# Kernel tuning notes

Measured on AMD Instinct MI355X. Metric: run time of the kernel, lower is better.

The kernel has to match this reference:

```python
import jax, jax.numpy as jnp
import numpy as np

N_NODES = 50000
N_EDGES = 600000
D = 128
NEG_SLOPE = (1.0 / 8.0 + 1.0 / 3.0) / 2.0  # RReLU in eval mode: mean of (lower, upper)


def setup_inputs() -> dict:
    key = jax.random.key(0)
    ks = jax.random.split(key, 16)
    inp = {
        'node_feats': jax.random.normal(ks[0], (N_NODES, D), dtype=jnp.float32),
        'edge_feats': jax.random.normal(ks[1], (N_EDGES, D), dtype=jnp.float32),
        'src': jax.random.randint(ks[2], (N_EDGES,), 0, N_NODES, dtype=jnp.int32),
        'dst': jax.random.randint(ks[3], (N_EDGES,), 0, N_NODES, dtype=jnp.int32),
    }
    scale = 1.0 / np.sqrt(D)
    i = 4
    for l in range(2):
        for w in (1, 2, 3):
            inp[f'W{w}_l{l}'] = jax.random.uniform(ks[i], (D, D), jnp.float32, -scale, scale); i += 1
            inp[f'b{w}_l{l}'] = jnp.zeros((D,), jnp.float32)
    return inp


def _layer(h, efeat, src, dst, W1, b1, W2, b2, W3, b3):
    # per-edge message: linear1(src_h + edge_h)  [E, D]
    m = (h[src] + efeat) @ W1 + b1
    # attention score per edge: <h_dst, m_e>
    score = jnp.sum(h[dst] * m, axis=-1)  # [E]
    smax = jax.ops.segment_max(score, dst, num_segments=N_NODES)
    smax = jnp.where(jnp.isfinite(smax), smax, 0.0)
    w = jnp.exp(score - smax[dst])  # [E]
    denom = jax.ops.segment_sum(w, dst, num_segments=N_NODES)  # [N]
    wsum = jax.ops.segment_sum(w[:, None] * m, dst, num_segments=N_NODES)  # [N, D]
    neigh = wsum / jnp.maximum(denom, 1e-30)[:, None]
    deg = jax.ops.segment_sum(jnp.ones_like(score), dst, num_segments=N_NODES)
    self_msg = h @ W2 + b2
    iso_msg = h @ W3 + b3
    self_msg = jnp.where((deg == 0)[:, None], iso_msg, self_msg)
    x = self_msg + neigh
    return jnp.where(x >= 0, x, x * NEG_SLOPE)


def reference(node_feats, edge_feats, src, dst,
              W1_l0, b1_l0, W2_l0, b2_l0, W3_l0, b3_l0,
              W1_l1, b1_l1, W2_l1, b2_l1, W3_l1, b3_l1):
    h = _layer(node_feats, edge_feats, src, dst, W1_l0, b1_l0, W2_l0, b2_l0, W3_l0, b3_l0)
    h = _layer(h, edge_feats, src, dst, W1_l1, b1_l1, W2_l1, b2_l1, W3_l1, b3_l1)
    return h
```

## Files before the change

kernel.cpp:

```cpp
#include <hip/hip_runtime.h>


typedef unsigned short u16;
typedef short bf16x8 __attribute__((ext_vector_type(8)));
typedef float f32x4 __attribute__((ext_vector_type(4)));

#define NEG_SLOPE 0.22916666666666666f

__device__ inline float bf2f(u16 h) { return __uint_as_float(((unsigned)h) << 16); }
__device__ inline u16 f2bf(float f) {
  unsigned u = __float_as_uint(f);
  u += 0x7fffu + ((u >> 16) & 1u);
  return (u16)(u >> 16);
}

__global__ __launch_bounds__(256)
void prep_weights(const float* w0, const float* w1, const float* w2,
                  const float* w3, const float* w4, const float* w5,
                  const float* c0, const float* c1, const float* c2,
                  const float* c3, const float* c4, const float* c5,
                  u16* __restrict__ wf, float* __restrict__ bf) {
  int bid = blockIdx.x, tid = threadIdx.x;
  int b = bid >> 3, qc = (bid & 7) * 8;
  const float* Ws[8] = {w0, w1, w2, w3, w4, w5, w0, w3};
  const float* Cs[6] = {c0, c1, c2, c3, c4, c5};
  const float* W = Ws[b];
  const bool tr = (b >= 6);
  u16* out = wf + (size_t)b * 32768;
  #pragma unroll
  for (int qq = 0; qq < 8; ++qq) {
    int fi = tid * 64 + qc + qq;
    int t = fi >> 11, kc = (fi >> 9) & 3, lane = (fi >> 3) & 63, j = fi & 7;
    int k = kc * 32 + (lane >> 4) * 8 + j;
    int n = t * 16 + (lane & 15);
    float w = tr ? W[n * 128 + k] : W[k * 128 + n];
    u16 hi = f2bf(w);
    u16 lo = f2bf(w - bf2f(hi));
    int base = ((t * 4 + kc) * 2) * 512 + lane * 8 + j;
    out[base] = hi;
    out[base + 512] = lo;
  }
  if ((bid & 7) == 0 && b < 6 && tid < 128) bf[b * 128 + tid] = Cs[b][tid];
}

__global__ __launch_bounds__(256)
void hist_k(const int* __restrict__ dst, int* __restrict__ deg, int E) {
  int i = blockIdx.x * 256 + threadIdx.x;
  int stride = gridDim.x * 256;
  for (; i < E; i += stride) atomicAdd(&deg[dst[i]], 1);
}

__global__ __launch_bounds__(256)
void scan1(const int* __restrict__ deg, int* __restrict__ off,
           int* __restrict__ bsum, int N) {
  __shared__ int sh[256];
  int b = blockIdx.x, t = threadIdx.x;
  int base = b * 1024 + t * 4;
  int v[4];
  #pragma unroll
  for (int i = 0; i < 4; ++i) v[i] = (base + i < N) ? deg[base + i] : 0;
  int s = v[0] + v[1] + v[2] + v[3];
  sh[t] = s;
  __syncthreads();
  for (int o = 1; o < 256; o <<= 1) {
    int x = (t >= o) ? sh[t - o] : 0;
    __syncthreads();
    sh[t] += x;
    __syncthreads();
  }
  int run = sh[t] - s;
  #pragma unroll
  for (int i = 0; i < 4; ++i) {
    if (base + i < N) off[base + i] = run;
    run += v[i];
  }
  if (t == 255) bsum[b] = sh[255];
}

__global__ void scan2(int* __restrict__ bsum, int nb) {
  __shared__ int sh[256];
  int t = threadIdx.x;
  int v = (t < nb) ? bsum[t] : 0;
  sh[t] = v;
  __syncthreads();
  for (int o = 1; o < 256; o <<= 1) {
    int x = (t >= o) ? sh[t - o] : 0;
    __syncthreads();
    sh[t] += x;
    __syncthreads();
  }
  if (t < nb) bsum[t] = sh[t] - v;
}

__global__ __launch_bounds__(256)
void scan3(int* __restrict__ off, const int* __restrict__ bsum,
           int* __restrict__ cursor, int N, int E) {
  int i = blockIdx.x * 256 + threadIdx.x;
  if (i < N) {
    int v = off[i] + bsum[i >> 10];
    off[i] = v;
    cursor[i] = v;
  } else if (i == N) {
    off[N] = E;
  }
}

__global__ __launch_bounds__(256)
void scatter_k(const int* __restrict__ dst, const int* __restrict__ src,
               int* __restrict__ cursor, int* __restrict__ eidx,
               int* __restrict__ csrc, int E) {
  int i = blockIdx.x * 256 + threadIdx.x;
  int stride = gridDim.x * 256;
  for (; i < E; i += stride) {
    int p = atomicAdd(&cursor[dst[i]], 1);
    eidx[p] = i;
    csrc[p] = src[i];
  }
}

__global__ __launch_bounds__(256)
void gemm_n3t(const float* __restrict__ A,
              const u16* __restrict__ wfT, const u16* __restrict__ wf2,
              const u16* __restrict__ wf3, const float* __restrict__ biases,
              float* __restrict__ C0, float* __restrict__ C1,
              float* __restrict__ C2, int M) {
  __shared__ u16 ah[64 * 136];
  __shared__ u16 al[64 * 136];
  const int tid = threadIdx.x;
  const long long rowBase = (long long)blockIdx.x * 64;
  #pragma unroll
  for (int it = 0; it < 8; ++it) {
    int idx = it * 256 + tid;
    int row = idx >> 5, c4 = idx & 31;
    long long gr = rowBase + row;
    float4 v = make_float4(0.f, 0.f, 0.f, 0.f);
    if (gr < M) v = ((const float4*)A)[gr * 32 + c4];
    u16 hb[4] = {f2bf(v.x), f2bf(v.y), f2bf(v.z), f2bf(v.w)};
    u16 lb[4] = {f2bf(v.x - bf2f(hb[0])), f2bf(v.y - bf2f(hb[1])),
                 f2bf(v.z - bf2f(hb[2])), f2bf(v.w - bf2f(hb[3]))};
    *(uint2*)&ah[row * 136 + c4 * 4] = *(uint2*)hb;
    *(uint2*)&al[row * 136 + c4 * 4] = *(uint2*)lb;
  }
  __syncthreads();
  const int wid = tid >> 6, lane = tid & 63, lrow = lane & 15, lk = lane >> 4;
  bf16x8 af[4], alf[4];
  #pragma unroll
  for (int kc = 0; kc < 4; ++kc) {
    af[kc]  = *(const bf16x8*)&ah[(wid * 16 + lrow) * 136 + kc * 32 + lk * 8];
    alf[kc] = *(const bf16x8*)&al[(wid * 16 + lrow) * 136 + kc * 32 + lk * 8];
  }
  const u16* wfs[3] = {wfT, wf2, wf3};
  float* Cs[3] = {C0, C1, C2};
  for (int m = 0; m < 3; ++m) {
    const u16* wf = wfs[m];
    float* C = Cs[m];
    f32x4 acc[8];
    #pragma unroll
    for (int t = 0; t < 8; ++t) acc[t] = (f32x4){0.f, 0.f, 0.f, 0.f};
    #pragma unroll
    for (int t = 0; t < 8; ++t) {
      #pragma unroll
      for (int kc = 0; kc < 4; ++kc) {
        bf16x8 bh = *(const bf16x8*)&wf[((t * 4 + kc) * 2) * 512 + lane * 8];
        bf16x8 bl = *(const bf16x8*)&wf[((t * 4 + kc) * 2 + 1) * 512 + lane * 8];
        acc[t] = __builtin_amdgcn_mfma_f32_16x16x32_bf16(af[kc],  bh, acc[t], 0, 0, 0);
        acc[t] = __builtin_amdgcn_mfma_f32_16x16x32_bf16(alf[kc], bh, acc[t], 0, 0, 0);
        acc[t] = __builtin_amdgcn_mfma_f32_16x16x32_bf16(af[kc],  bl, acc[t], 0, 0, 0);
      }
    }
    #pragma unroll
    for (int t = 0; t < 8; ++t) {
      int col = t * 16 + lrow;
      float bv = (m == 1) ? biases[128 + col] : (m == 2) ? biases[256 + col] : 0.f;
      #pragma unroll
      for (int r = 0; r < 4; ++r) {
        long long row = rowBase + wid * 16 + lk * 4 + r;
        if (row < M) C[row * 128 + col] = acc[t][r] + bv;
      }
    }
  }
}

__global__ __launch_bounds__(256)
void edge_agg(const float* __restrict__ efeat, const float* __restrict__ h,
              const float* __restrict__ hT1, const int* __restrict__ off,
              const int* __restrict__ eidx, const int* __restrict__ csrc,
              float* __restrict__ U, int N) {
  int node = blockIdx.x * 4 + (threadIdx.x >> 6);
  if (node >= N) return;
  const int lane = threadIdx.x & 63;
  const size_t nb = (size_t)node * 128 + 2 * lane;
  int s0 = off[node], s1 = off[node + 1];
  if (s1 == s0) {
    *(float2*)&U[nb] = make_float2(0.f, 0.f);
    return;
  }
  const float2 ht = *(const float2*)&hT1[nb];
  float mx = -3.4e38f, den = 0.f, ux = 0.f, uy = 0.f;
  for (int base = s0; base < s1; base += 64) {
    int cnt = s1 - base;
    if (cnt > 64) cnt = 64;
    int me = 0, ms = 0;
    if (lane < cnt) { me = eidx[base + lane]; ms = csrc[base + lane]; }
    int e0 = __shfl(me, 0), sA = __shfl(ms, 0);
    float2 ef = *(const float2*)&efeat[(size_t)e0 * 128 + 2 * lane];
    float2 hs = *(const float2*)&h[(size_t)sA * 128 + 2 * lane];
    for (int j = 0; j < cnt; ++j) {
      float vx = ef.x + hs.x, vy = ef.y + hs.y;
      if (j + 1 < cnt) {
        int e1 = __shfl(me, j + 1), sB = __shfl(ms, j + 1);
        ef = *(const float2*)&efeat[(size_t)e1 * 128 + 2 * lane];
        hs = *(const float2*)&h[(size_t)sB * 128 + 2 * lane];
      }
      float psum = vx * ht.x + vy * ht.y;
      #pragma unroll
      for (int o = 32; o > 0; o >>= 1) psum += __shfl_xor(psum, o);
      if (psum > mx) {
        float r = __expf(mx - psum);
        den *= r; ux *= r; uy *= r;
        mx = psum;
      }
      float w = __expf(psum - mx);
      den += w;
      ux += w * vx; uy += w * vy;
    }
  }
  float inv = 1.f / den;
  *(float2*)&U[nb] = make_float2(ux * inv, uy * inv);
}

__global__ __launch_bounds__(256)
void gemm_fin(const float* __restrict__ A,
              const u16* __restrict__ wf,
              const float* __restrict__ biases,
              const float* __restrict__ y2, const float* __restrict__ y3,
              const int* __restrict__ off, float* __restrict__ C, int M) {
  __shared__ u16 ah[64 * 136];
  __shared__ u16 al[64 * 136];
  const int tid = threadIdx.x;
  const long long rowBase = (long long)blockIdx.x * 64;
  #pragma unroll
  for (int it = 0; it < 8; ++it) {
    int idx = it * 256 + tid;
    int row = idx >> 5, c4 = idx & 31;
    long long gr = rowBase + row;
    float4 v = make_float4(0.f, 0.f, 0.f, 0.f);
    if (gr < M) v = ((const float4*)A)[gr * 32 + c4];
    u16 hb[4] = {f2bf(v.x), f2bf(v.y), f2bf(v.z), f2bf(v.w)};
    u16 lb[4] = {f2bf(v.x - bf2f(hb[0])), f2bf(v.y - bf2f(hb[1])),
                 f2bf(v.z - bf2f(hb[2])), f2bf(v.w - bf2f(hb[3]))};
    *(uint2*)&ah[row * 136 + c4 * 4] = *(uint2*)hb;
    *(uint2*)&al[row * 136 + c4 * 4] = *(uint2*)lb;
  }
  __syncthreads();
  const int wid = tid >> 6, lane = tid & 63, lrow = lane & 15, lk = lane >> 4;
  bf16x8 af[4], alf[4];
  #pragma unroll
  for (int kc = 0; kc < 4; ++kc) {
    af[kc]  = *(const bf16x8*)&ah[(wid * 16 + lrow) * 136 + kc * 32 + lk * 8];
    alf[kc] = *(const bf16x8*)&al[(wid * 16 + lrow) * 136 + kc * 32 + lk * 8];
  }
  f32x4 acc[8];
  #pragma unroll
  for (int t = 0; t < 8; ++t) acc[t] = (f32x4){0.f, 0.f, 0.f, 0.f};
  #pragma unroll
  for (int t = 0; t < 8; ++t) {
    #pragma unroll
    for (int kc = 0; kc < 4; ++kc) {
      bf16x8 bh = *(const bf16x8*)&wf[((t * 4 + kc) * 2) * 512 + lane * 8];
      bf16x8 bl = *(const bf16x8*)&wf[((t * 4 + kc) * 2 + 1) * 512 + lane * 8];
      acc[t] = __builtin_amdgcn_mfma_f32_16x16x32_bf16(af[kc],  bh, acc[t], 0, 0, 0);
      acc[t] = __builtin_amdgcn_mfma_f32_16x16x32_bf16(alf[kc], bh, acc[t], 0, 0, 0);
      acc[t] = __builtin_amdgcn_mfma_f32_16x16x32_bf16(af[kc],  bl, acc[t], 0, 0, 0);
    }
  }
  #pragma unroll
  for (int r = 0; r < 4; ++r) {
    long long row = rowBase + wid * 16 + lk * 4 + r;
    if (row >= M) continue;
    int dg = off[row + 1] - off[row];
    #pragma unroll
    for (int t = 0; t < 8; ++t) {
      int col = t * 16 + lrow;
      size_t o = (size_t)row * 128 + col;
      float v;
      if (dg) v = acc[t][r] + y2[o] + biases[col];
      else    v = y3[o];
      v = v >= 0.f ? v : v * NEG_SLOPE;
      C[o] = v;
    }
  }
}

extern "C" void kernel_launch(void* const* d_in, const int* in_sizes, int n_in,
                              void* d_out, int out_size, void* d_ws, size_t ws_size,
                              hipStream_t stream) {
  const int D = 128;
  const int N = in_sizes[0] / D;
  const int E = in_sizes[1] / D;

  const float* node  = (const float*)d_in[0];
  const float* edgef = (const float*)d_in[1];
  const int* src = (const int*)d_in[2];
  const int* dst = (const int*)d_in[3];

  char* p = (char*)d_ws;
  u16*   wfrag = (u16*)p;   p += (size_t)8 * 32768 * 2;
  float* biasf = (float*)p; p += 4096;
  float* hT1   = (float*)p; p += (size_t)N * 512;
  float* y2    = (float*)p; p += (size_t)N * 512;
  float* y3    = (float*)p; p += (size_t)N * 512;
  float* h1    = (float*)p; p += (size_t)N * 512;
  float* Ub    = (float*)p; p += (size_t)N * 512;
  int* deg     = (int*)p;   p += (size_t)N * 4;
  int* off     = (int*)p;   p += (size_t)(N + 256) * 4;
  int* cursor  = (int*)p;   p += (size_t)N * 4;
  int* bsum    = (int*)p;   p += 1024;
  int* eidx    = (int*)p;   p += (size_t)E * 4;
  int* csrc    = (int*)p;   p += (size_t)E * 4;
  (void)ws_size;

  prep_weights<<<64, 256, 0, stream>>>(
      (const float*)d_in[4],  (const float*)d_in[6],  (const float*)d_in[8],
      (const float*)d_in[10], (const float*)d_in[12], (const float*)d_in[14],
      (const float*)d_in[5],  (const float*)d_in[7],  (const float*)d_in[9],
      (const float*)d_in[11], (const float*)d_in[13], (const float*)d_in[15],
      wfrag, biasf);

  const int gN = (N + 63) / 64;
  const int eB = (E + 255) / 256;
  const int nb = (N + 1023) / 1024;

  hipMemsetAsync(deg, 0, (size_t)N * 4, stream);
  hist_k<<<eB, 256, 0, stream>>>(dst, deg, E);
  scan1<<<nb, 256, 0, stream>>>(deg, off, bsum, N);
  scan2<<<1, 256, 0, stream>>>(bsum, nb);
  scan3<<<(N + 256) / 256, 256, 0, stream>>>(off, bsum, cursor, N, E);
  scatter_k<<<eB, 256, 0, stream>>>(dst, src, cursor, eidx, csrc, E);

  for (int l = 0; l < 2; ++l) {
    const float* h = (l == 0) ? node : h1;
    float* hout = (l == 0) ? h1 : (float*)d_out;
    const u16* wf1 = wfrag + (size_t)(l * 3 + 0) * 32768;
    const u16* wf2 = wfrag + (size_t)(l * 3 + 1) * 32768;
    const u16* wf3 = wfrag + (size_t)(l * 3 + 2) * 32768;
    const u16* wfT = wfrag + (size_t)(6 + l) * 32768;
    const float* bset = biasf + l * 384;

    gemm_n3t<<<gN, 256, 0, stream>>>(h, wfT, wf2, wf3, bset, hT1, y2, y3, N);
    edge_agg<<<(N + 3) / 4, 256, 0, stream>>>(edgef, h, hT1, off, eidx, csrc,
                                              Ub, N);
    gemm_fin<<<gN, 256, 0, stream>>>(Ub, wf1, bset, y2, y3, off, hout, N);
  }
}
```

Before: 892.6 us.

## Process four edges per wave in edge aggregation and skip unused iso GEMM

The edge aggregation kernel now splits each 64-lane wave into four 16-lane groups. Each group handles a different edge, loads 8 floats per lane with nontemporal edge-feature loads, and prefetches indices two steps ahead. An online softmax merges the group maxima and partial sums each step, and the partials are reduced across groups at the end. This cuts the serial per-edge shuffle-reduction chain and raises memory-level parallelism. Separately, the node GEMM skips computing the isolated-node projection for 64-row tiles that contain no zero-degree nodes, which adds an extra pass over the offsets plus a barrier.

Result: faster. 797.7 us (-10.6%).

```diff
diff --git a/kernel.cpp b/kernel.cpp
--- a/kernel.cpp
+++ b/kernel.cpp
@@ -122,12 +122,16 @@
 void gemm_n3t(const float* __restrict__ A,
               const u16* __restrict__ wfT, const u16* __restrict__ wf2,
               const u16* __restrict__ wf3, const float* __restrict__ biases,
+              const int* __restrict__ off,
               float* __restrict__ C0, float* __restrict__ C1,
               float* __restrict__ C2, int M) {
   __shared__ u16 ah[64 * 136];
   __shared__ u16 al[64 * 136];
+  __shared__ int anyDeg0;
   const int tid = threadIdx.x;
   const long long rowBase = (long long)blockIdx.x * 64;
+  if (tid == 0) anyDeg0 = 0;
+  __syncthreads();
   #pragma unroll
   for (int it = 0; it < 8; ++it) {
     int idx = it * 256 + tid;
@@ -141,7 +145,12 @@
     *(uint2*)&ah[row * 136 + c4 * 4] = *(uint2*)hb;
     *(uint2*)&al[row * 136 + c4 * 4] = *(uint2*)lb;
   }
+  if (tid < 64) {
+    long long r = rowBase + tid;
+    if (r < M && off[r + 1] == off[r]) anyDeg0 = 1;
+  }
   __syncthreads();
+  const int nsets = anyDeg0 ? 3 : 2;
   const int wid = tid >> 6, lane = tid & 63, lrow = lane & 15, lk = lane >> 4;
   bf16x8 af[4], alf[4];
   #pragma unroll
@@ -151,7 +160,7 @@
   }
   const u16* wfs[3] = {wfT, wf2, wf3};
   float* Cs[3] = {C0, C1, C2};
-  for (int m = 0; m < 3; ++m) {
+  for (int m = 0; m < nsets; ++m) {
     const u16* wf = wfs[m];
     float* C = Cs[m];
     f32x4 acc[8];
@@ -189,44 +198,83 @@
   int node = blockIdx.x * 4 + (threadIdx.x >> 6);
   if (node >= N) return;
   const int lane = threadIdx.x & 63;
-  const size_t nb = (size_t)node * 128 + 2 * lane;
-  int s0 = off[node], s1 = off[node + 1];
-  if (s1 == s0) {
-    *(float2*)&U[nb] = make_float2(0.f, 0.f);
+  const int g = lane >> 4, cl = lane & 15;
+  const size_t nb = (size_t)node * 128 + (size_t)cl * 8;
+  const int s0 = off[node];
+  const int cnt = off[node + 1] - s0;
+  if (cnt == 0) {
+    if (g == 0) {
+      *(f32x4*)&U[nb]     = (f32x4){0.f, 0.f, 0.f, 0.f};
+      *(f32x4*)&U[nb + 4] = (f32x4){0.f, 0.f, 0.f, 0.f};
+    }
     return;
   }
-  const float2 ht = *(const float2*)&hT1[nb];
-  float mx = -3.4e38f, den = 0.f, ux = 0.f, uy = 0.f;
-  for (int base = s0; base < s1; base += 64) {
-    int cnt = s1 - base;
-    if (cnt > 64) cnt = 64;
-    int me = 0, ms = 0;
-    if (lane < cnt) { me = eidx[base + lane]; ms = csrc[base + lane]; }
-    int e0 = __shfl(me, 0), sA = __shfl(ms, 0);
-    float2 ef = *(const float2*)&efeat[(size_t)e0 * 128 + 2 * lane];
-    float2 hs = *(const float2*)&h[(size_t)sA * 128 + 2 * lane];
-    for (int j = 0; j < cnt; ++j) {
-      float vx = ef.x + hs.x, vy = ef.y + hs.y;
-      if (j + 1 < cnt) {
-        int e1 = __shfl(me, j + 1), sB = __shfl(ms, j + 1);
-        ef = *(const float2*)&efeat[(size_t)e1 * 128 + 2 * lane];
-        hs = *(const float2*)&h[(size_t)sB * 128 + 2 * lane];
-      }
-      float psum = vx * ht.x + vy * ht.y;
-      #pragma unroll
-      for (int o = 32; o > 0; o >>= 1) psum += __shfl_xor(psum, o);
-      if (psum > mx) {
-        float r = __expf(mx - psum);
-        den *= r; ux *= r; uy *= r;
-        mx = psum;
-      }
-      float w = __expf(psum - mx);
-      den += w;
-      ux += w * vx; uy += w * vy;
-    }
+  const f32x4 ht0 = *(const f32x4*)&hT1[nb];
+  const f32x4 ht1 = *(const f32x4*)&hT1[nb + 4];
+  float mx = -3.4e38f, den = 0.f;
+  f32x4 u0 = (f32x4){0.f, 0.f, 0.f, 0.f};
+  f32x4 u1 = (f32x4){0.f, 0.f, 0.f, 0.f};
+  const int nsteps = (cnt + 3) >> 2;
+
+  bool actC = (g < cnt);
+  {
+    int i0 = s0 + (actC ? g : 0);
+    int eC = eidx[i0], sC = csrc[i0];
+    const f32x4* efp = (const f32x4*)(efeat + (size_t)eC * 128) + cl * 2;
+    const f32x4* hp  = (const f32x4*)(h + (size_t)sC * 128) + cl * 2;
+    f32x4 fC0 = __builtin_nontemporal_load(efp);
+    f32x4 fC1 = __builtin_nontemporal_load(efp + 1);
+    f32x4 hC0 = hp[0], hC1 = hp[1];
+
+    int j1 = 4 + g;
+    bool actN = (j1 < cnt);
+    int i1 = s0 + (actN ? j1 : 0);
+    int eN = eidx[i1], sN = csrc[i1];
+
+    for (int k = 0; k < nsteps; ++k) {
+      const f32x4* efn = (const f32x4*)(efeat + (size_t)eN * 128) + cl * 2;
+      const f32x4* hn  = (const f32x4*)(h + (size_t)sN * 128) + cl * 2;
+      f32x4 fN0 = __builtin_nontemporal_load(efn);
+      f32x4 fN1 = __builtin_nontemporal_load(efn + 1);
+      f32x4 hN0 = hn[0], hN1 = hn[1];
+      int j2 = (k + 2) * 4 + g;
+      bool act2 = (j2 < cnt);
+      int i2 = s0 + (act2 ? j2 : 0);
+      int e2 = eidx[i2], s2 = csrc[i2];
+
+      f32x4 v0 = fC0 + hC0, v1 = fC1 + hC1;
+      float ps = v0[0] * ht0[0] + v0[1] * ht0[1] + v0[2] * ht0[2] + v0[3] * ht0[3]
+               + v1[0] * ht1[0] + v1[1] * ht1[1] + v1[2] * ht1[2] + v1[3] * ht1[3];
+      ps += __shfl_xor(ps, 1);
+      ps += __shfl_xor(ps, 2);
+      ps += __shfl_xor(ps, 4);
+      ps += __shfl_xor(ps, 8);
+      float s = actC ? ps : -3.4e38f;
+      float m2 = fmaxf(s, __shfl_xor(s, 16));
+      float m4 = fmaxf(m2, __shfl_xor(m2, 32));
+      float mxn = fmaxf(mx, m4);
+      float r = __expf(mx - mxn);
+      float w = __expf(s - mxn);
+      float w2 = w + __shfl_xor(w, 16);
+      float w4 = w2 + __shfl_xor(w2, 32);
+      den = den * r + w4;
+      u0 = u0 * r + w * v0;
+      u1 = u1 * r + w * v1;
+      mx = mxn;
+      fC0 = fN0; fC1 = fN1; hC0 = hN0; hC1 = hN1; actC = actN;
+      eN = e2; sN = s2; actN = act2;
+    }
+  }
+  #pragma unroll
+  for (int c = 0; c < 4; ++c) {
+    u0[c] += __shfl_xor(u0[c], 16); u0[c] += __shfl_xor(u0[c], 32);
+    u1[c] += __shfl_xor(u1[c], 16); u1[c] += __shfl_xor(u1[c], 32);
   }
   float inv = 1.f / den;
-  *(float2*)&U[nb] = make_float2(ux * inv, uy * inv);
+  if (g == 0) {
+    *(f32x4*)&U[nb]     = u0 * inv;
+    *(f32x4*)&U[nb + 4] = u1 * inv;
+  }
 }
 
 __global__ __launch_bounds__(256)
@@ -347,7 +395,7 @@
     const u16* wfT = wfrag + (size_t)(6 + l) * 32768;
     const float* bset = biasf + l * 384;
 
-    gemm_n3t<<<gN, 256, 0, stream>>>(h, wfT, wf2, wf3, bset, hT1, y2, y3, N);
+    gemm_n3t<<<gN, 256, 0, stream>>>(h, wfT, wf2, wf3, bset, off, hT1, y2, y3, N);
     edge_agg<<<(N + 3) / 4, 256, 0, stream>>>(edgef, h, hT1, off, eidx, csrc,
                                               Ub, N);
     gemm_fin<<<gN, 256, 0, stream>>>(Ub, wf1, bset, y2, y3, off, hout, N);
```

## Restructure edge aggregation to 16 lanes per node with 4-deep prefetch

Applied to the files above, without the earlier changes.

The edge aggregation kernel now assigns 16 lanes per node instead of a full 64-lane wavefront. Each lane handles 8 features with 128-bit loads, and four edges stay in flight through a software-pipelined prefetch ring using nontemporal loads for edge features. The (edge, src) indices are packed into one int2 array so each edge needs a single index load. The node GEMM also skips the isolated-node weight product for tiles with no zero-degree node. The online softmax defers rescaling until the max grows by more than 8, which trades a small risk of reduced exp range for fewer rescales, and packing 4 nodes per wave can cause divergence when degrees differ.

Result: faster. 797.1 us (-10.7%).

```diff
diff --git a/kernel.cpp b/kernel.cpp
--- a/kernel.cpp
+++ b/kernel.cpp
@@ -107,14 +107,12 @@
 
 __global__ __launch_bounds__(256)
 void scatter_k(const int* __restrict__ dst, const int* __restrict__ src,
-               int* __restrict__ cursor, int* __restrict__ eidx,
-               int* __restrict__ csrc, int E) {
+               int* __restrict__ cursor, int2* __restrict__ epair, int E) {
   int i = blockIdx.x * 256 + threadIdx.x;
   int stride = gridDim.x * 256;
   for (; i < E; i += stride) {
     int p = atomicAdd(&cursor[dst[i]], 1);
-    eidx[p] = i;
-    csrc[p] = src[i];
+    epair[p] = make_int2(i, src[i]);
   }
 }
 
@@ -122,12 +120,16 @@
 void gemm_n3t(const float* __restrict__ A,
               const u16* __restrict__ wfT, const u16* __restrict__ wf2,
               const u16* __restrict__ wf3, const float* __restrict__ biases,
+              const int* __restrict__ off,
               float* __restrict__ C0, float* __restrict__ C1,
               float* __restrict__ C2, int M) {
   __shared__ u16 ah[64 * 136];
   __shared__ u16 al[64 * 136];
+  __shared__ int anyDeg0;
   const int tid = threadIdx.x;
   const long long rowBase = (long long)blockIdx.x * 64;
+  if (tid == 0) anyDeg0 = 0;
+  __syncthreads();
   #pragma unroll
   for (int it = 0; it < 8; ++it) {
     int idx = it * 256 + tid;
@@ -141,7 +143,12 @@
     *(uint2*)&ah[row * 136 + c4 * 4] = *(uint2*)hb;
     *(uint2*)&al[row * 136 + c4 * 4] = *(uint2*)lb;
   }
-  __syncthreads();
+  if (tid < 64) {
+    long long r = rowBase + tid;
+    if (r < M && off[r + 1] == off[r]) anyDeg0 = 1;
+  }
+  __syncthreads();
+  const int nsets = anyDeg0 ? 3 : 2;
   const int wid = tid >> 6, lane = tid & 63, lrow = lane & 15, lk = lane >> 4;
   bf16x8 af[4], alf[4];
   #pragma unroll
@@ -151,7 +158,7 @@
   }
   const u16* wfs[3] = {wfT, wf2, wf3};
   float* Cs[3] = {C0, C1, C2};
-  for (int m = 0; m < 3; ++m) {
+  for (int m = 0; m < nsets; ++m) {
     const u16* wf = wfs[m];
     float* C = Cs[m];
     f32x4 acc[8];
@@ -184,49 +191,86 @@
 __global__ __launch_bounds__(256)
 void edge_agg(const float* __restrict__ efeat, const float* __restrict__ h,
               const float* __restrict__ hT1, const int* __restrict__ off,
-              const int* __restrict__ eidx, const int* __restrict__ csrc,
-              float* __restrict__ U, int N) {
-  int node = blockIdx.x * 4 + (threadIdx.x >> 6);
-  if (node >= N) return;
-  const int lane = threadIdx.x & 63;
-  const size_t nb = (size_t)node * 128 + 2 * lane;
-  int s0 = off[node], s1 = off[node + 1];
-  if (s1 == s0) {
-    *(float2*)&U[nb] = make_float2(0.f, 0.f);
-    return;
-  }
-  const float2 ht = *(const float2*)&hT1[nb];
-  float mx = -3.4e38f, den = 0.f, ux = 0.f, uy = 0.f;
-  for (int base = s0; base < s1; base += 64) {
-    int cnt = s1 - base;
-    if (cnt > 64) cnt = 64;
-    int me = 0, ms = 0;
-    if (lane < cnt) { me = eidx[base + lane]; ms = csrc[base + lane]; }
-    int e0 = __shfl(me, 0), sA = __shfl(ms, 0);
-    float2 ef = *(const float2*)&efeat[(size_t)e0 * 128 + 2 * lane];
-    float2 hs = *(const float2*)&h[(size_t)sA * 128 + 2 * lane];
-    for (int j = 0; j < cnt; ++j) {
-      float vx = ef.x + hs.x, vy = ef.y + hs.y;
-      if (j + 1 < cnt) {
-        int e1 = __shfl(me, j + 1), sB = __shfl(ms, j + 1);
-        ef = *(const float2*)&efeat[(size_t)e1 * 128 + 2 * lane];
-        hs = *(const float2*)&h[(size_t)sB * 128 + 2 * lane];
-      }
-      float psum = vx * ht.x + vy * ht.y;
-      #pragma unroll
-      for (int o = 32; o > 0; o >>= 1) psum += __shfl_xor(psum, o);
-      if (psum > mx) {
-        float r = __expf(mx - psum);
-        den *= r; ux *= r; uy *= r;
-        mx = psum;
-      }
-      float w = __expf(psum - mx);
-      den += w;
-      ux += w * vx; uy += w * vy;
-    }
-  }
-  float inv = 1.f / den;
-  *(float2*)&U[nb] = make_float2(ux * inv, uy * inv);
+              const int2* __restrict__ epair, float* __restrict__ U, int N) {
+  const int node = blockIdx.x * 16 + (threadIdx.x >> 4);
+  const int cl = threadIdx.x & 15;
+  const bool valid = (node < N);
+  const size_t nb = (size_t)node * 128 + (size_t)cl * 8;
+  int s0 = 0, cnt = 0;
+  if (valid) {
+    s0 = off[node];
+    cnt = off[node + 1] - s0;
+  }
+  int jm = cnt;
+  jm = max(jm, __shfl_xor(jm, 16));
+  jm = max(jm, __shfl_xor(jm, 32));
+
+  f32x4 ht0 = (f32x4){0.f, 0.f, 0.f, 0.f}, ht1 = ht0;
+  if (valid && cnt > 0) {
+    ht0 = *(const f32x4*)&hT1[nb];
+    ht1 = *(const f32x4*)&hT1[nb + 4];
+  }
+
+  f32x4 fA0, fA1, hA0, hA1, fB0, fB1, hB0, hB1;
+  f32x4 fC0, fC1, hC0, hC1, fD0, fD1, hD0, hD1;
+  int2 iA = make_int2(0, 0), iB = iA, iC = iA, iD = iA;
+
+  #define PRO(S, JJ)                                                          \
+    if (JJ < cnt) {                                                           \
+      int2 pr = epair[s0 + JJ];                                               \
+      const f32x4* efp = (const f32x4*)(efeat + (size_t)pr.x * 128) + cl * 2; \
+      f##S##0 = __builtin_nontemporal_load(efp);                              \
+      f##S##1 = __builtin_nontemporal_load(efp + 1);                          \
+      const f32x4* hp = (const f32x4*)(h + (size_t)pr.y * 128) + cl * 2;      \
+      h##S##0 = hp[0]; h##S##1 = hp[1];                                       \
+      if (JJ + 4 < cnt) i##S = epair[s0 + JJ + 4];                            \
+    }
+  PRO(A, 0) PRO(B, 1) PRO(C, 2) PRO(D, 3)
+  #undef PRO
+
+  float mx = -3.4e38f, den = 0.f;
+  f32x4 u0 = (f32x4){0.f, 0.f, 0.f, 0.f}, u1 = u0;
+
+  #define PROC(S, OFS) {                                                      \
+    int je = j + OFS;                                                         \
+    if (je < cnt) {                                                           \
+      f32x4 v0 = f##S##0 + h##S##0, v1 = f##S##1 + h##S##1;                   \
+      float ps = v0[0]*ht0[0] + v0[1]*ht0[1] + v0[2]*ht0[2] + v0[3]*ht0[3]    \
+               + v1[0]*ht1[0] + v1[1]*ht1[1] + v1[2]*ht1[2] + v1[3]*ht1[3];   \
+      ps += __shfl_xor(ps, 1); ps += __shfl_xor(ps, 2);                       \
+      ps += __shfl_xor(ps, 4); ps += __shfl_xor(ps, 8);                       \
+      if (ps > mx + 8.f) {                                                    \
+        float rr = __expf(mx - ps);           \
+        den *= rr; u0 *= rr; u1 *= rr; mx = ps;                               \
+      }                                                                       \
+      float w = __expf(ps - mx);                          \
+      den += w; u0 += w * v0; u1 += w * v1;                                   \
+      int jr = je + 4;                                                        \
+      if (jr < cnt) {                                                         \
+        const f32x4* efp = (const f32x4*)(efeat + (size_t)i##S.x * 128) + cl * 2; \
+        f##S##0 = __builtin_nontemporal_load(efp);                            \
+        f##S##1 = __builtin_nontemporal_load(efp + 1);                        \
+        const f32x4* hp = (const f32x4*)(h + (size_t)i##S.y * 128) + cl * 2;  \
+        h##S##0 = hp[0]; h##S##1 = hp[1];                                     \
+        if (je + 8 < cnt) i##S = epair[s0 + je + 8];                          \
+      }                                                                       \
+    }                                                                         \
+  }
+  for (int j = 0; j < jm; j += 4) {
+    PROC(A, 0) PROC(B, 1) PROC(C, 2) PROC(D, 3)
+  }
+  #undef PROC
+
+  if (valid) {
+    if (cnt == 0) {
+      *(f32x4*)&U[nb]     = (f32x4){0.f, 0.f, 0.f, 0.f};
+      *(f32x4*)&U[nb + 4] = (f32x4){0.f, 0.f, 0.f, 0.f};
+    } else {
+      float inv = 1.f / den;
+      *(f32x4*)&U[nb]     = u0 * inv;
+      *(f32x4*)&U[nb + 4] = u1 * inv;
+    }
+  }
 }
 
 __global__ __launch_bounds__(256)
@@ -316,8 +360,7 @@
   int* off     = (int*)p;   p += (size_t)(N + 256) * 4;
   int* cursor  = (int*)p;   p += (size_t)N * 4;
   int* bsum    = (int*)p;   p += 1024;
-  int* eidx    = (int*)p;   p += (size_t)E * 4;
-  int* csrc    = (int*)p;   p += (size_t)E * 4;
+  int2* epair  = (int2*)p;  p += (size_t)E * 8;
   (void)ws_size;
 
   prep_weights<<<64, 256, 0, stream>>>(
@@ -336,7 +379,7 @@
   scan1<<<nb, 256, 0, stream>>>(deg, off, bsum, N);
   scan2<<<1, 256, 0, stream>>>(bsum, nb);
   scan3<<<(N + 256) / 256, 256, 0, stream>>>(off, bsum, cursor, N, E);
-  scatter_k<<<eB, 256, 0, stream>>>(dst, src, cursor, eidx, csrc, E);
+  scatter_k<<<eB, 256, 0, stream>>>(dst, src, cursor, epair, E);
 
   for (int l = 0; l < 2; ++l) {
     const float* h = (l == 0) ? node : h1;
@@ -347,9 +390,8 @@
     const u16* wfT = wfrag + (size_t)(6 + l) * 32768;
     const float* bset = biasf + l * 384;
 
-    gemm_n3t<<<gN, 256, 0, stream>>>(h, wfT, wf2, wf3, bset, hT1, y2, y3, N);
-    edge_agg<<<(N + 3) / 4, 256, 0, stream>>>(edgef, h, hT1, off, eidx, csrc,
-                                              Ub, N);
+    gemm_n3t<<<gN, 256, 0, stream>>>(h, wfT, wf2, wf3, bset, off, hT1, y2, y3, N);
+    edge_agg<<<(N + 15) / 16, 256, 0, stream>>>(edgef, h, hT1, off, epair, Ub, N);
     gemm_fin<<<gN, 256, 0, stream>>>(Ub, wf1, bset, y2, y3, off, hout, N);
   }
 }
```
